# Kernel tuning notes

Measured on AMD Instinct MI355X. Metric: run time of the kernel, lower is better.

The kernel has to match this reference:

```python
import jax, jax.numpy as jnp
import numpy as np

H, KV, D = 32, 8, 128  # n_head, n_head_kv, head_dim
HID = 4096


def setup_inputs() -> dict:
    key = jax.random.key(0)
    ks = jax.random.split(key, 6)
    B, Q, P = 4, 1024, 1024  # batch, new tokens, past cache len
    return {
        "input_t": jax.random.normal(ks[0], (B, Q, HID), jnp.float32),
        "key_cache": jax.random.normal(ks[1], (B, P, KV, D), jnp.float32),
        "value_cache": jax.random.normal(ks[2], (B, P, KV, D), jnp.float32),
        "max_position": 2048,
        "attention_mask": jnp.zeros((B, 1, Q, P + Q), jnp.float32),
        "beam_idx": jnp.zeros((B,), jnp.int32),
        "qkv_w": jax.random.normal(ks[3], ((H + 2 * KV) * D, HID), jnp.float32) * 0.02,
        "qkv_b": jnp.zeros(((H + 2 * KV) * D,), jnp.float32),
    }


def reference(input_t, key_cache, value_cache, max_position, attention_mask, beam_idx, qkv_w, qkv_b):
    B, Q, _ = input_t.shape
    n_rep = H // KV
    fused = input_t @ qkv_w.T + qkv_b  # [B,Q,(H+2KV)*D]
    q = fused[..., : H * D].reshape(B, Q, H, D)
    k_new = fused[..., H * D : (H + KV) * D].reshape(B, Q, KV, D)
    v_new = fused[..., (H + KV) * D :].reshape(B, Q, KV, D)
    k = jnp.concatenate([key_cache, k_new], axis=1)    # [B,S,KV,D]
    v = jnp.concatenate([value_cache, v_new], axis=1)  # [B,S,KV,D]
    # GQA: group query heads per kv head instead of materializing repeated KV
    qg = q.reshape(B, Q, KV, n_rep, D)
    scores = jnp.einsum("bqkrd,bskd->bkrqs", qg, k) / (D ** 0.5)
    scores = scores + attention_mask[:, :, None]  # [B,1,1,Q,S] broadcast
    probs = jax.nn.softmax(scores, axis=-1)
    out = jnp.einsum("bkrqs,bskd->bkrqd", probs, v).reshape(B, KV * n_rep, Q, D)
    return out, k, v
```

## Files before the change

kernel.cpp:

```cpp
#include <hip/hip_runtime.h>


typedef __attribute__((ext_vector_type(4))) float f32x4;
typedef __attribute__((ext_vector_type(8))) short bf16x8;
typedef __attribute__((ext_vector_type(8))) unsigned short u16x8;
typedef __attribute__((ext_vector_type(4))) unsigned short u16x4;

#define LOG2E 1.4426950408889634f
#define SCALE 0.08838834764831843f
#define SCALE2 0.12751649736689687f

__device__ __forceinline__ unsigned short f2bf(float f) {
  unsigned int u = __builtin_bit_cast(unsigned int, f);
  u = (u + 0x7FFFu + ((u >> 16) & 1u)) >> 16;
  return (unsigned short)u;
}

__device__ __forceinline__ void async16(void* lds, const void* g) {
  __builtin_amdgcn_global_load_lds(
      (const __attribute__((address_space(1))) unsigned int*)(unsigned long long)g,
      (__attribute__((address_space(3))) unsigned int*)(unsigned int)(unsigned long long)lds,
      16, 0, 0);
}


__global__ __launch_bounds__(256) void conv_bf16_kernel(
    const float* __restrict__ in, unsigned short* __restrict__ out, int n8) {
  int i = blockIdx.x * 256 + threadIdx.x;
  if (i >= n8) return;
  const f32x4* in4 = (const f32x4*)in;
  f32x4 a = in4[i * 2], c = in4[i * 2 + 1];
  u16x8 o;
#pragma unroll
  for (int j = 0; j < 4; j++) { o[j] = f2bf(a[j]); o[4 + j] = f2bf(c[j]); }
  *(u16x8*)(out + i * 8) = o;
}

__global__ __launch_bounds__(256) void conv_k_kernel(
    const float* __restrict__ kc, unsigned short* __restrict__ Kb, float* __restrict__ outK) {
  int i = blockIdx.x * 256 + threadIdx.x;
  int d8 = i & 15, kv = (i >> 4) & 7, s = (i >> 7) & 1023, b = i >> 17;
  const float* src = kc + (((b * 1024 + s) * 8 + kv) * 128) + d8 * 8;
  f32x4 v0 = ((const f32x4*)src)[0], v1 = ((const f32x4*)src)[1];
  float* ko = outK + (((b * 2048 + s) * 8 + kv) * 128) + d8 * 8;
  ((f32x4*)ko)[0] = v0; ((f32x4*)ko)[1] = v1;
  u16x8 o;
#pragma unroll
  for (int j = 0; j < 4; j++) { o[j] = f2bf(v0[j]); o[4 + j] = f2bf(v1[j]); }
  *(u16x8*)(Kb + ((b * 8 + kv) * 2048 + s) * 128 + d8 * 8) = o;
}

__global__ __launch_bounds__(256) void conv_v_kernel(
    const float* __restrict__ vc, unsigned short* __restrict__ Vtb, float* __restrict__ outV) {
  __shared__ unsigned short t[32][33];
  const int bid = blockIdx.x;
  const int s0 = (bid & 31) * 32;
  const int d0 = ((bid >> 5) & 3) * 32;
  const int kv = (bid >> 7) & 7;
  const int b = bid >> 10;
  const int tx = threadIdx.x & 31, ty = threadIdx.x >> 5;
#pragma unroll
  for (int p = 0; p < 4; p++) {
    const int si = p * 8 + ty;
    float v = vc[(((b * 1024 + s0 + si) * 8 + kv) * 128) + d0 + tx];
    outV[(((b * 2048 + s0 + si) * 8 + kv) * 128) + d0 + tx] = v;
    t[tx][si] = f2bf(v);
  }
  __syncthreads();
#pragma unroll
  for (int p = 0; p < 4; p++) {
    const int dr = p * 8 + ty;
    Vtb[((b * 8 + kv) * 128 + d0 + dr) * 2048 + s0 + tx] = t[dr][tx];
  }
}

__global__ __launch_bounds__(256) void qkv_gemm_kernel(
    const unsigned short* __restrict__ Xb, const unsigned short* __restrict__ Wb,
    const float* __restrict__ bias,
    unsigned short* __restrict__ Qb, unsigned short* __restrict__ Kb,
    unsigned short* __restrict__ Vtb, float* __restrict__ outK, float* __restrict__ outV) {
  const int K = 4096;
  __shared__ unsigned short As[4096];
  __shared__ unsigned short Bs[4096];
  const int tid = threadIdx.x;
  const int wave = tid >> 6, lane = tid & 63;
  const int g = lane >> 4, l15 = lane & 15;
  const int flat = blockIdx.x + gridDim.x * blockIdx.y;
  const int swz = (flat & 7) * 192 + (flat >> 3);
  const int bm = swz & 31, bn = swz >> 5;
  const int wr = wave >> 1, wc = wave & 1;

  const int slot0 = wave * 128 + lane, slot1 = slot0 + 64;
  const int r0 = slot0 >> 2, c0 = (slot0 & 3) ^ ((r0 >> 1) & 3);
  const int r1 = slot1 >> 2, c1 = (slot1 & 3) ^ ((r1 >> 1) & 3);

  const unsigned short* Ab = Xb + bm * 128 * K;
  const unsigned short* Bb = Wb + bn * 128 * K;
  const unsigned short* gA0 = Ab + r0 * K + c0 * 8;
  const unsigned short* gA1 = Ab + r1 * K + c1 * 8;
  const unsigned short* gB0 = Bb + r0 * K + c0 * 8;
  const unsigned short* gB1 = Bb + r1 * K + c1 * 8;
  unsigned short* ldsA0 = As + wave * 1024;
  unsigned short* ldsA1 = As + wave * 1024 + 512;
  unsigned short* ldsB0 = Bs + wave * 1024;
  unsigned short* ldsB1 = Bs + wave * 1024 + 512;

  f32x4 acc[4][4] = {};

  for (int k0 = 0; k0 < K; k0 += 32) {
    async16(ldsA0, gA0 + k0);
    async16(ldsA1, gA1 + k0);
    async16(ldsB0, gB0 + k0);
    async16(ldsB1, gB1 + k0);
    __syncthreads();
    bf16x8 af[4], bfr[4];
#pragma unroll
    for (int i = 0; i < 4; i++) {
      const int rm = wr * 64 + i * 16 + l15;
      af[i] = *(const bf16x8*)(As + rm * 32 + ((g ^ ((rm >> 1) & 3)) * 8));
      const int rn = wc * 64 + i * 16 + l15;
      bfr[i] = *(const bf16x8*)(Bs + rn * 32 + ((g ^ ((rn >> 1) & 3)) * 8));
    }
#pragma unroll
    for (int i = 0; i < 4; i++)
#pragma unroll
      for (int j = 0; j < 4; j++)
        acc[i][j] = __builtin_amdgcn_mfma_f32_16x16x32_bf16(af[i], bfr[j], acc[i][j], 0, 0, 0);
    __syncthreads();
  }

  const int b = bm >> 3;
  const int qbase = (bm & 7) << 7;
  if (bn < 32) {
#pragma unroll
    for (int j = 0; j < 4; j++) {
      const int n = bn * 128 + wc * 64 + j * 16 + l15;
      const float bv = bias[n];
      const int h = n >> 7, d = n & 127;
#pragma unroll
      for (int i = 0; i < 4; i++) {
        const int q0 = qbase + wr * 64 + i * 16 + g * 4;
        unsigned short* dst = Qb + (((b * 32 + h) * 1024 + q0) * 128 + d);
#pragma unroll
        for (int r = 0; r < 4; r++) dst[r * 128] = f2bf(acc[i][j][r] + bv);
      }
    }
  } else if (bn < 40) {
#pragma unroll
    for (int j = 0; j < 4; j++) {
      const int n = bn * 128 + wc * 64 + j * 16 + l15;
      const float bv = bias[n];
      const int n2 = n - 4096, kv = n2 >> 7, d = n2 & 127;
#pragma unroll
      for (int i = 0; i < 4; i++) {
        const int q0 = qbase + wr * 64 + i * 16 + g * 4;
        float* ko = outK + (((b * 2048 + 1024 + q0) * 8 + kv) * 128 + d);
        unsigned short* kb = Kb + (((b * 8 + kv) * 2048 + 1024 + q0) * 128 + d);
#pragma unroll
        for (int r = 0; r < 4; r++) {
          float v = acc[i][j][r] + bv;
          ko[r * 1024] = v;
          kb[r * 128] = f2bf(v);
        }
      }
    }
  } else {
#pragma unroll
    for (int j = 0; j < 4; j++) {
      const int n = bn * 128 + wc * 64 + j * 16 + l15;
      const float bv = bias[n];
      const int n2 = n - 5120, kv = n2 >> 7, d = n2 & 127;
#pragma unroll
      for (int i = 0; i < 4; i++) {
        const int q0 = qbase + wr * 64 + i * 16 + g * 4;
        float* vo = outV + (((b * 2048 + 1024 + q0) * 8 + kv) * 128 + d);
        u16x4 pk;
#pragma unroll
        for (int r = 0; r < 4; r++) {
          float v = acc[i][j][r] + bv;
          vo[r * 1024] = v;
          pk[r] = f2bf(v);
        }
        *(u16x4*)(Vtb + ((b * 8 + kv) * 128 + d) * 2048 + 1024 + q0) = pk;
      }
    }
  }
}

__global__ __launch_bounds__(256) void attn_kernel(
    const unsigned short* __restrict__ Qb, const unsigned short* __restrict__ Kb,
    const unsigned short* __restrict__ Vtb, const float* __restrict__ mask,
    float* __restrict__ outO) {
  __shared__ unsigned short Ks[64 * 128];
  __shared__ unsigned short Vs[128 * 64];
  __shared__ unsigned short Ps[4][32 * 80];

  const int tid = threadIdx.x, wave = tid >> 6, lane = tid & 63;
  const int g = lane >> 4, l15 = lane & 15;
  const int qt = blockIdx.x, h = blockIdx.y, b = blockIdx.z;
  const int kvh = h >> 2;

  const unsigned short* Kg = Kb + (b * 8 + kvh) * 2048 * 128;
  const unsigned short* Vg = Vtb + (b * 8 + kvh) * 128 * 2048;
  const int qg0 = qt * 128 + wave * 32;

  bf16x8 qf[2][4];
#pragma unroll
  for (int i = 0; i < 2; i++) {
    const unsigned short* qrow = Qb + (((b * 32 + h) * 1024) + qg0 + i * 16 + l15) * 128;
#pragma unroll
    for (int kg = 0; kg < 4; kg++) qf[i][kg] = *(const bf16x8*)(qrow + kg * 32 + g * 8);
  }

  f32x4 acc_o[2][8] = {};
  float m_run[2] = {-1e30f, -1e30f}, l_run[2] = {0.f, 0.f};

  unsigned short* Pw = Ps[wave];
  const int sbB = (lane & 48) | (g << 2);

  for (int s0 = 0; s0 < 2048; s0 += 64) {
    __syncthreads();
#pragma unroll
    for (int j = 0; j < 4; j++) {
      const int ksl = (j * 4 + wave) * 64 + lane;
      const int kr = ksl >> 4, kp = ksl & 15;
      async16(Ks + (j * 4 + wave) * 512, Kg + (s0 + kr) * 128 + ((kp ^ (kr & 7)) * 8));
      const int vd = ksl >> 3, vp = ksl & 7;
      async16(Vs + (j * 4 + wave) * 512, Vg + vd * 2048 + s0 + ((vp ^ (vd & 7)) * 8));
    }
    __syncthreads();

    f32x4 scv[2][4];
#pragma unroll
    for (int st = 0; st < 4; st++) {
      bf16x8 kfr[4];
      const int row = st * 16 + l15;
#pragma unroll
      for (int kg = 0; kg < 4; kg++)
        kfr[kg] = *(const bf16x8*)(Ks + row * 128 + (((kg * 4 + g) ^ (row & 7)) * 8));
#pragma unroll
      for (int i = 0; i < 2; i++) {
        f32x4 a = {};
#pragma unroll
        for (int kg = 0; kg < 4; kg++)
          a = __builtin_amdgcn_mfma_f32_16x16x32_bf16(kfr[kg], qf[i][kg], a, 0, 0, 0);
        scv[i][st] = a;
      }
    }

    float alpha_bc[2][4];
#pragma unroll
    for (int i = 0; i < 2; i++) {
      const float* mrow = mask + ((b * 1024 + qg0 + i * 16 + l15) * 2048) + s0;
      f32x4 x[4];
#pragma unroll
      for (int st = 0; st < 4; st++) {
        const f32x4 mv = *(const f32x4*)(mrow + st * 16 + g * 4);
#pragma unroll
        for (int r = 0; r < 4; r++) x[st][r] = scv[i][st][r] * SCALE2 + mv[r] * LOG2E;
      }
      float mx = x[0][0];
#pragma unroll
      for (int st = 0; st < 4; st++)
#pragma unroll
        for (int r = 0; r < 4; r++) mx = fmaxf(mx, x[st][r]);
      mx = fmaxf(mx, __shfl_xor(mx, 16));
      mx = fmaxf(mx, __shfl_xor(mx, 32));
      const float mnew = fmaxf(m_run[i], mx);
      const float al = exp2f(m_run[i] - mnew);
      m_run[i] = mnew;
      float ps = 0.f;
#pragma unroll
      for (int st = 0; st < 4; st++) {
        u16x4 pk;
#pragma unroll
        for (int r = 0; r < 4; r++) {
          const float p = exp2f(x[st][r] - mnew);
          ps += p;
          pk[r] = f2bf(p);
        }
        *(u16x4*)(Pw + (i * 16 + l15) * 80 + st * 16 + g * 4) = pk;
      }
      ps += __shfl_xor(ps, 16);
      ps += __shfl_xor(ps, 32);
      l_run[i] = l_run[i] * al + ps;
#pragma unroll
      for (int r = 0; r < 4; r++) alpha_bc[i][r] = __shfl(al, sbB + r);
    }

#pragma unroll
    for (int i = 0; i < 2; i++)
#pragma unroll
      for (int ds = 0; ds < 8; ds++)
#pragma unroll
        for (int r = 0; r < 4; r++) acc_o[i][ds][r] *= alpha_bc[i][r];

    bf16x8 pf[2][2];
#pragma unroll
    for (int i = 0; i < 2; i++)
#pragma unroll
      for (int ks = 0; ks < 2; ks++)
        pf[i][ks] = *(const bf16x8*)(Pw + (i * 16 + l15) * 80 + ks * 32 + g * 8);
#pragma unroll
    for (int ds = 0; ds < 8; ds++) {
      const int dr = ds * 16 + l15;
#pragma unroll
      for (int ks = 0; ks < 2; ks++) {
        bf16x8 vf = *(const bf16x8*)(Vs + dr * 64 + (((ks * 4 + g) ^ (dr & 7)) * 8));
#pragma unroll
        for (int i = 0; i < 2; i++)
          acc_o[i][ds] = __builtin_amdgcn_mfma_f32_16x16x32_bf16(pf[i][ks], vf, acc_o[i][ds], 0, 0, 0);
      }
    }
  }

#pragma unroll
  for (int i = 0; i < 2; i++) {
    const float invl = 1.0f / l_run[i];
#pragma unroll
    for (int r = 0; r < 4; r++) {
      const float inv = __shfl(invl, sbB + r);
      const int qgl = qg0 + i * 16 + g * 4 + r;
      float* orow = outO + (((b * 32 + h) * 1024) + qgl) * 128 + l15;
#pragma unroll
      for (int ds = 0; ds < 8; ds++) orow[ds * 16] = acc_o[i][ds][r] * inv;
    }
  }
}


extern "C" void kernel_launch(void* const* d_in, const int* in_sizes, int n_in,
                              void* d_out, int out_size, void* d_ws, size_t ws_size,
                              hipStream_t stream) {
  const float* input_t = (const float*)d_in[0];
  const float* key_cache = (const float*)d_in[1];
  const float* value_cache = (const float*)d_in[2];
  const float* attn_mask = (const float*)d_in[4];
  const float* qkv_w = (const float*)d_in[6];
  const float* qkv_b = (const float*)d_in[7];

  float* out = (float*)d_out;
  float* outK = out + 16777216;
  float* outV = outK + 8388608;

  char* ws = (char*)d_ws;
  unsigned short* Xb = (unsigned short*)ws;
  unsigned short* Wb = (unsigned short*)(ws + 33554432);
  unsigned short* Qb = (unsigned short*)(ws + 83886080);
  unsigned short* Kb = (unsigned short*)(ws + 117440512);
  unsigned short* Vtb = (unsigned short*)(ws + 134217728);

  hipLaunchKernelGGL(conv_bf16_kernel, dim3(8192), dim3(256), 0, stream, input_t, Xb, 2097152);
  hipLaunchKernelGGL(conv_bf16_kernel, dim3(12288), dim3(256), 0, stream, qkv_w, Wb, 3145728);
  hipLaunchKernelGGL(conv_k_kernel, dim3(2048), dim3(256), 0, stream, key_cache, Kb, outK);
  hipLaunchKernelGGL(conv_v_kernel, dim3(4096), dim3(256), 0, stream, value_cache, Vtb, outV);
  hipLaunchKernelGGL(qkv_gemm_kernel, dim3(32, 48), dim3(256), 0, stream,
                     Xb, Wb, qkv_b, Qb, Kb, Vtb, outK, outV);
  hipLaunchKernelGGL(attn_kernel, dim3(8, 32, 4), dim3(256), 0, stream,
                     Qb, Kb, Vtb, attn_mask, out);
}
```

Before: 1.112 ms.

## Double-buffer K/V tiles, enlarge attention blocks, and pass probabilities via bpermute

The attention kernel now uses 512-thread blocks covering 256 query rows and double-buffered K/V shared-memory tiles. The next tile is prefetched asynchronously while the current one is computed, leaving one barrier per iteration instead of two. Probabilities are packed with v_cvt_pk_bf16 and rearranged with ds_bpermute rather than going through LDS. The online-softmax rescale is skipped when the new max stays within 8 (log2 units) of the running max. This removes LDS round-trips and load stalls but raises register pressure and makes larger unnormalized exponent values possible.

```diff
diff --git a/kernel.cpp b/kernel.cpp
--- a/kernel.cpp
+++ b/kernel.cpp
@@ -5,15 +5,21 @@
 typedef __attribute__((ext_vector_type(8))) short bf16x8;
 typedef __attribute__((ext_vector_type(8))) unsigned short u16x8;
 typedef __attribute__((ext_vector_type(4))) unsigned short u16x4;
+typedef __attribute__((ext_vector_type(4))) unsigned int u32x4;
 
 #define LOG2E 1.4426950408889634f
-#define SCALE 0.08838834764831843f
 #define SCALE2 0.12751649736689687f
 
 __device__ __forceinline__ unsigned short f2bf(float f) {
   unsigned int u = __builtin_bit_cast(unsigned int, f);
   u = (u + 0x7FFFu + ((u >> 16) & 1u)) >> 16;
   return (unsigned short)u;
+}
+
+__device__ __forceinline__ int cvtpk_bf16(float lo, float hi) {
+  int d;
+  asm("v_cvt_pk_bf16_f32 %0, %1, %2" : "=v"(d) : "v"(lo), "v"(hi));
+  return d;
 }
 
 __device__ __forceinline__ void async16(void* lds, const void* g) {
@@ -187,13 +193,12 @@
   }
 }
 
-__global__ __launch_bounds__(256) void attn_kernel(
+__global__ __launch_bounds__(512, 2) void attn_kernel(
     const unsigned short* __restrict__ Qb, const unsigned short* __restrict__ Kb,
     const unsigned short* __restrict__ Vtb, const float* __restrict__ mask,
     float* __restrict__ outO) {
-  __shared__ unsigned short Ks[64 * 128];
-  __shared__ unsigned short Vs[128 * 64];
-  __shared__ unsigned short Ps[4][32 * 80];
+  __shared__ unsigned short Ks[2][8192];
+  __shared__ unsigned short Vs[2][8192];
 
   const int tid = threadIdx.x, wave = tid >> 6, lane = tid & 63;
   const int g = lane >> 4, l15 = lane & 15;
@@ -202,7 +207,7 @@
 
   const unsigned short* Kg = Kb + (b * 8 + kvh) * 2048 * 128;
   const unsigned short* Vg = Vtb + (b * 8 + kvh) * 128 * 2048;
-  const int qg0 = qt * 128 + wave * 32;
+  const int qg0 = qt * 256 + wave * 32;
 
   bf16x8 qf[2][4];
 #pragma unroll
@@ -215,20 +220,41 @@
   f32x4 acc_o[2][8] = {};
   float m_run[2] = {-1e30f, -1e30f}, l_run[2] = {0.f, 0.f};
 
-  unsigned short* Pw = Ps[wave];
   const int sbB = (lane & 48) | (g << 2);
-
-  for (int s0 = 0; s0 < 2048; s0 += 64) {
-    __syncthreads();
-#pragma unroll
-    for (int j = 0; j < 4; j++) {
-      const int ksl = (j * 4 + wave) * 64 + lane;
-      const int kr = ksl >> 4, kp = ksl & 15;
-      async16(Ks + (j * 4 + wave) * 512, Kg + (s0 + kr) * 128 + ((kp ^ (kr & 7)) * 8));
-      const int vd = ksl >> 3, vp = ksl & 7;
-      async16(Vs + (j * 4 + wave) * 512, Vg + vd * 2048 + s0 + ((vp ^ (vd & 7)) * 8));
-    }
-    __syncthreads();
+  const int srcA4 = ((lane & 15) | ((lane & 16) << 1)) << 2;
+  const int srcB4 = srcA4 + 64;
+  const bool hi32 = (lane & 32) != 0;
+
+  {
+#pragma unroll
+    for (int j = 0; j < 2; j++) {
+      const int region = j * 8 + wave;
+      const int slot = region * 64 + lane;
+      const int kr = slot >> 4, kp = slot & 15;
+      async16(&Ks[0][region * 512], Kg + kr * 128 + ((kp ^ (kr & 7)) * 8));
+      const int vd = slot >> 3, vp = slot & 7;
+      async16(&Vs[0][region * 512], Vg + vd * 2048 + ((vp ^ (vd & 7)) * 8));
+    }
+  }
+  __syncthreads();
+
+  for (int t = 0; t < 32; t++) {
+    const int cb = t & 1;
+    const unsigned short* Kc = Ks[cb];
+    const unsigned short* Vc = Vs[cb];
+    if (t < 31) {
+      const int s1 = (t + 1) * 64;
+#pragma unroll
+      for (int j = 0; j < 2; j++) {
+        const int region = j * 8 + wave;
+        const int slot = region * 64 + lane;
+        const int kr = slot >> 4, kp = slot & 15;
+        async16(&Ks[cb ^ 1][region * 512], Kg + (s1 + kr) * 128 + ((kp ^ (kr & 7)) * 8));
+        const int vd = slot >> 3, vp = slot & 7;
+        async16(&Vs[cb ^ 1][region * 512], Vg + vd * 2048 + s1 + ((vp ^ (vd & 7)) * 8));
+      }
+    }
+    const int s0 = t * 64;
 
     f32x4 scv[2][4];
 #pragma unroll
@@ -237,7 +263,7 @@
       const int row = st * 16 + l15;
 #pragma unroll
       for (int kg = 0; kg < 4; kg++)
-        kfr[kg] = *(const bf16x8*)(Ks + row * 128 + (((kg * 4 + g) ^ (row & 7)) * 8));
+        kfr[kg] = *(const bf16x8*)(Kc + row * 128 + (((kg * 4 + g) ^ (row & 7)) * 8));
 #pragma unroll
       for (int i = 0; i < 2; i++) {
         f32x4 a = {};
@@ -248,70 +274,96 @@
       }
     }
 
-    float alpha_bc[2][4];
+    float mx[2];
+    f32x4 x[2][4];
 #pragma unroll
     for (int i = 0; i < 2; i++) {
       const float* mrow = mask + ((b * 1024 + qg0 + i * 16 + l15) * 2048) + s0;
-      f32x4 x[4];
 #pragma unroll
       for (int st = 0; st < 4; st++) {
         const f32x4 mv = *(const f32x4*)(mrow + st * 16 + g * 4);
 #pragma unroll
-        for (int r = 0; r < 4; r++) x[st][r] = scv[i][st][r] * SCALE2 + mv[r] * LOG2E;
-      }
-      float mx = x[0][0];
+        for (int r = 0; r < 4; r++) x[i][st][r] = scv[i][st][r] * SCALE2 + mv[r] * LOG2E;
+      }
+      float m0 = x[i][0][0];
 #pragma unroll
       for (int st = 0; st < 4; st++)
 #pragma unroll
-        for (int r = 0; r < 4; r++) mx = fmaxf(mx, x[st][r]);
-      mx = fmaxf(mx, __shfl_xor(mx, 16));
-      mx = fmaxf(mx, __shfl_xor(mx, 32));
-      const float mnew = fmaxf(m_run[i], mx);
-      const float al = exp2f(m_run[i] - mnew);
-      m_run[i] = mnew;
+        for (int r = 0; r < 4; r++) m0 = fmaxf(m0, x[i][st][r]);
+      m0 = fmaxf(m0, __shfl_xor(m0, 16));
+      m0 = fmaxf(m0, __shfl_xor(m0, 32));
+      mx[i] = m0;
+    }
+
+    const int skip = __all((mx[0] <= m_run[0] + 8.0f) & (mx[1] <= m_run[1] + 8.0f));
+
+    int pk[2][4][2];
+#pragma unroll
+    for (int i = 0; i < 2; i++) {
+      float mnew = m_run[i], al = 1.0f;
+      if (!skip) {
+        mnew = fmaxf(m_run[i], mx[i]);
+        al = exp2f(m_run[i] - mnew);
+        m_run[i] = mnew;
+      }
       float ps = 0.f;
 #pragma unroll
       for (int st = 0; st < 4; st++) {
-        u16x4 pk;
-#pragma unroll
-        for (int r = 0; r < 4; r++) {
-          const float p = exp2f(x[st][r] - mnew);
-          ps += p;
-          pk[r] = f2bf(p);
-        }
-        *(u16x4*)(Pw + (i * 16 + l15) * 80 + st * 16 + g * 4) = pk;
+        float p0 = exp2f(x[i][st][0] - mnew);
+        float p1 = exp2f(x[i][st][1] - mnew);
+        float p2 = exp2f(x[i][st][2] - mnew);
+        float p3 = exp2f(x[i][st][3] - mnew);
+        ps += (p0 + p1) + (p2 + p3);
+        pk[i][st][0] = cvtpk_bf16(p0, p1);
+        pk[i][st][1] = cvtpk_bf16(p2, p3);
       }
       ps += __shfl_xor(ps, 16);
       ps += __shfl_xor(ps, 32);
       l_run[i] = l_run[i] * al + ps;
-#pragma unroll
-      for (int r = 0; r < 4; r++) alpha_bc[i][r] = __shfl(al, sbB + r);
-    }
-
+      if (!skip) {
+#pragma unroll
+        for (int r = 0; r < 4; r++) {
+          const float ab = __shfl(al, sbB + r);
+#pragma unroll
+          for (int ds = 0; ds < 8; ds++) acc_o[i][ds][r] *= ab;
+        }
+      }
+    }
+
+    bf16x8 pf[2][2];
 #pragma unroll
     for (int i = 0; i < 2; i++)
 #pragma unroll
-      for (int ds = 0; ds < 8; ds++)
-#pragma unroll
-        for (int r = 0; r < 4; r++) acc_o[i][ds][r] *= alpha_bc[i][r];
-
-    bf16x8 pf[2][2];
-#pragma unroll
-    for (int i = 0; i < 2; i++)
-#pragma unroll
-      for (int ks = 0; ks < 2; ks++)
-        pf[i][ks] = *(const bf16x8*)(Pw + (i * 16 + l15) * 80 + ks * 32 + g * 8);
+      for (int ks = 0; ks < 2; ks++) {
+        const int a0 = __builtin_amdgcn_ds_bpermute(srcA4, pk[i][2 * ks][0]);
+        const int b0 = __builtin_amdgcn_ds_bpermute(srcA4, pk[i][2 * ks + 1][0]);
+        const int a1 = __builtin_amdgcn_ds_bpermute(srcA4, pk[i][2 * ks][1]);
+        const int b1 = __builtin_amdgcn_ds_bpermute(srcA4, pk[i][2 * ks + 1][1]);
+        const int a2 = __builtin_amdgcn_ds_bpermute(srcB4, pk[i][2 * ks][0]);
+        const int b2 = __builtin_amdgcn_ds_bpermute(srcB4, pk[i][2 * ks + 1][0]);
+        const int a3 = __builtin_amdgcn_ds_bpermute(srcB4, pk[i][2 * ks][1]);
+        const int b3 = __builtin_amdgcn_ds_bpermute(srcB4, pk[i][2 * ks + 1][1]);
+        u32x4 dw;
+        dw[0] = (unsigned)(hi32 ? b0 : a0);
+        dw[1] = (unsigned)(hi32 ? b1 : a1);
+        dw[2] = (unsigned)(hi32 ? b2 : a2);
+        dw[3] = (unsigned)(hi32 ? b3 : a3);
+        pf[i][ks] = __builtin_bit_cast(bf16x8, dw);
+      }
+
 #pragma unroll
     for (int ds = 0; ds < 8; ds++) {
       const int dr = ds * 16 + l15;
 #pragma unroll
       for (int ks = 0; ks < 2; ks++) {
-        bf16x8 vf = *(const bf16x8*)(Vs + dr * 64 + (((ks * 4 + g) ^ (dr & 7)) * 8));
+        bf16x8 vf = *(const bf16x8*)(Vc + dr * 64 + (((ks * 4 + g) ^ (dr & 7)) * 8));
 #pragma unroll
         for (int i = 0; i < 2; i++)
           acc_o[i][ds] = __builtin_amdgcn_mfma_f32_16x16x32_bf16(pf[i][ks], vf, acc_o[i][ds], 0, 0, 0);
       }
     }
+
+    __syncthreads();
   }
 
 #pragma unroll
@@ -356,6 +408,6 @@
   hipLaunchKernelGGL(conv_v_kernel, dim3(4096), dim3(256), 0, stream, value_cache, Vtb, outV);
   hipLaunchKernelGGL(qkv_gemm_kernel, dim3(32, 48), dim3(256), 0, stream,
                      Xb, Wb, qkv_b, Qb, Kb, Vtb, outK, outV);
-  hipLaunchKernelGGL(attn_kernel, dim3(8, 32, 4), dim3(256), 0, stream,
+  hipLaunchKernelGGL(attn_kernel, dim3(4, 32, 4), dim3(512), 0, stream,
                      Qb, Kb, Vtb, attn_mask, out);
 }
```

Measured after the change: 928.6 us. -16.5%, faster.
